# Kernel optimization log

Hardware: AMD Instinct MI355X
Metric: run time of the kernel (lower is better)

Reference implementation:

```python
import jax, jax.numpy as jnp
import numpy as np

SP, WD, H, HID = 8, 3, 8, 256
D = HID // H
TEMP = 0.1


def setup_inputs() -> dict:
    key = jax.random.key(0)
    ks = jax.random.split(key, 14)
    B, Lq, Lk, F = 4, 1024, 2048, SP + WD
    s = 0.05
    return {
        "q_fp": jax.random.normal(ks[0], (B, Lq, F), jnp.float32),
        "v_ret": jax.random.normal(ks[1], (B, Lk, F), jnp.float32),
        "pi_star": jax.random.uniform(ks[2], (B, Lq, Lk), jnp.float32),
        "Wq_s": jax.random.normal(ks[3], (HID, SP), jnp.float32) * s,
        "bq_s": jax.random.normal(ks[4], (HID,), jnp.float32) * s,
        "Wk_s": jax.random.normal(ks[5], (HID, SP), jnp.float32) * s,
        "bk_s": jax.random.normal(ks[6], (HID,), jnp.float32) * s,
        "Wq_w": jax.random.normal(ks[7], (HID, WD), jnp.float32) * s,
        "bq_w": jax.random.normal(ks[8], (HID,), jnp.float32) * s,
        "Wk_w": jax.random.normal(ks[9], (HID, WD), jnp.float32) * s,
        "bk_w": jax.random.normal(ks[10], (HID,), jnp.float32) * s,
        "Wv": jax.random.normal(ks[11], (HID, F), jnp.float32) * s,
        "bv": jnp.zeros((HID,), jnp.float32),
        "Wo": jax.random.normal(ks[12], (HID, HID), jnp.float32) * s,
        "bo": jnp.zeros((HID,), jnp.float32),
        "wave_blend": jnp.array(0.5, jnp.float32),
    }


def _proj(x, W, b):
    # x: [B, L, F_in] -> [B, H, L, D]
    B, L, _ = x.shape
    return (x @ W.T + b).reshape(B, L, H, D).transpose(0, 2, 1, 3)


def reference(q_fp, v_ret, pi_star, Wq_s, bq_s, Wk_s, bk_s, Wq_w, bq_w, Wk_w, bk_w, Wv, bv, Wo, bo, wave_blend):
    B, Lq, _ = q_fp.shape
    # split streams: first SP dims spatial, next WD dims wave (F == SP+WD)
    q_sp, q_wv = q_fp[..., :SP], q_fp[..., SP:SP + WD]
    k_sp, k_wv = v_ret[..., :SP], v_ret[..., SP:SP + WD]
    # structural branch: scaled dot product
    q_struct = _proj(q_sp, Wq_s, bq_s)
    k_struct = _proj(k_sp, Wk_s, bk_s)
    spatial_logits = jnp.einsum('bhqd,bhkd->bhqk', q_struct, k_struct) / np.float32(np.sqrt(D))
    # wave branch: negative squared euclidean distance via norm expansion
    q_wp = _proj(q_wv, Wq_w, bq_w)
    k_wp = _proj(k_wv, Wk_w, bk_w)
    qn = jnp.sum(q_wp * q_wp, axis=-1)[..., :, None]   # [B,H,Lq,1]
    kn = jnp.sum(k_wp * k_wp, axis=-1)[..., None, :]   # [B,H,1,Lk]
    qk = jnp.einsum('bhqd,bhkd->bhqk', q_wp, k_wp)
    wave_logits = -(qn + kn - 2.0 * qk) / np.float32(TEMP)
    alpha = jax.nn.sigmoid(wave_blend)
    transport_mask = jnp.log(jnp.clip(pi_star, 1e-9, None))[:, None]  # [B,1,Lq,Lk]
    attn = jax.nn.softmax((1.0 - alpha) * spatial_logits + alpha * wave_logits + transport_mask, axis=-1)
    values = _proj(v_ret, Wv, bv)  # [B,H,Lk,D]
    ctx = jnp.einsum('bhqk,bhkd->bhqd', attn, values)
    ctx = ctx.transpose(0, 2, 1, 3).reshape(B, Lq, HID)
    return ctx @ Wo.T + bo
```

## Files before the change

kernel.cpp:

```cpp
#include <hip/hip_runtime.h>
#include <hip/hip_bf16.h>
#include <cstdint>

#define B_    4
#define LQ    1024
#define LK    2048
#define FEAT  11
#define SP_   8
#define WD_   3
#define H_    8
#define HID_  256
#define LOG2E 1.4426950408889634f
#define SPLIT 4
#define KPS   (LK / SPLIT)
#define ITERS (KPS / 64)

typedef __attribute__((ext_vector_type(4))) float f32x4;
typedef __attribute__((ext_vector_type(8))) short bf16x8;
typedef __attribute__((ext_vector_type(4))) short s16x4;

__device__ __forceinline__ float sigmoidf_(float x) { return 1.f / (1.f + __expf(-x)); }

__device__ __forceinline__ short f2bf(float f) {
  unsigned u = __float_as_uint(f);
  u += 0x7fffu + ((u >> 16) & 1u);
  return (short)(u >> 16);
}
__device__ __forceinline__ float bf2f(short s) {
  return __uint_as_float(((unsigned)(unsigned short)s) << 16);
}

__device__ __forceinline__ void gl_lds16(const void* g, void* l) {
  __builtin_amdgcn_global_load_lds(
      (const __attribute__((address_space(1))) unsigned int*)g,
      (__attribute__((address_space(3))) unsigned int*)l, 16, 0, 0);
}

__global__ __launch_bounds__(256) void proj_q_kernel(
    const float* __restrict__ q_fp, const float* __restrict__ Wq_s,
    const float* __restrict__ bq_s, const float* __restrict__ Wq_w,
    const float* __restrict__ bq_w, const float* __restrict__ wb,
    short* __restrict__ Qh)
{
  const int row = blockIdx.x;
  const int t   = threadIdx.x;
  const float alpha = sigmoidf_(wb[0]);
  const float c1 = (1.f - alpha) * 0.17677669529663687f * LOG2E;
  const float c2 = 2.f * alpha * 10.f * LOG2E;

  const float* x = q_fp + (size_t)row * FEAT;
  float xs[FEAT];
  #pragma unroll
  for (int f = 0; f < FEAT; ++f) xs[f] = x[f];

  float s = bq_s[t];
  #pragma unroll
  for (int f = 0; f < SP_; ++f) s += xs[f] * Wq_s[t * SP_ + f];
  float w = bq_w[t];
  #pragma unroll
  for (int f = 0; f < WD_; ++f) w += xs[SP_ + f] * Wq_w[t * WD_ + f];

  const int h = t >> 5, d = t & 31;
  const int b = row >> 10, q = row & (LQ - 1);
  const size_t base = ((size_t)(b * H_ + h) * LQ + q) * 64;
  Qh[base + d]      = f2bf(c1 * s);
  Qh[base + 32 + d] = f2bf(c2 * w);
}

__global__ __launch_bounds__(256) void projk_pack_kernel(
    const float* __restrict__ v_ret, const float* __restrict__ Wk_s,
    const float* __restrict__ bk_s, const float* __restrict__ Wk_w,
    const float* __restrict__ bk_w, const float* __restrict__ Wv,
    const float* __restrict__ bv,   const float* __restrict__ wb,
    short* __restrict__ KV, float* __restrict__ kb)
{
  __shared__ float ldsv[64][33];
  const int blk = blockIdx.x, bh = blockIdx.y;
  const int b = bh >> 3, h = bh & 7;
  const int t = threadIdx.x;
  const int kl = t >> 2, part = t & 3;
  const int k = blk * 64 + kl;
  const float alpha = sigmoidf_(wb[0]);

  const float* x = v_ret + (size_t)(b * LK + k) * FEAT;
  float xs[FEAT];
  #pragma unroll
  for (int f = 0; f < FEAT; ++f) xs[f] = x[f];

  float s8[8], w8[8], v8[8];
  #pragma unroll
  for (int i = 0; i < 8; ++i) {
    const int d = h * 32 + part * 8 + i;
    float s = bk_s[d];
    #pragma unroll
    for (int f = 0; f < SP_; ++f) s += xs[f] * Wk_s[d * SP_ + f];
    float w = bk_w[d];
    #pragma unroll
    for (int f = 0; f < WD_; ++f) w += xs[SP_ + f] * Wk_w[d * WD_ + f];
    float v = bv[d];
    #pragma unroll
    for (int f = 0; f < FEAT; ++f) v += xs[f] * Wv[d * FEAT + f];
    s8[i] = s; w8[i] = w; v8[i] = v;
    ldsv[kl][part * 8 + i] = v;
  }

  float sq = 0.f;
  #pragma unroll
  for (int i = 0; i < 8; ++i) sq += w8[i] * w8[i];
  sq += __shfl_xor(sq, 1);
  sq += __shfl_xor(sq, 2);
  if (part == 0) kb[(size_t)bh * LK + k] = -10.f * alpha * LOG2E * sq;

  const int a  = kl >> 5;
  const int bb = (kl >> 2) & 1;
  const int p  = kl - a * 32 - bb * 4;
  const int lo = ((p >> 3) << 2) | (p & 3);
  const int t4 = a * 2 + bb;
  const size_t base = ((size_t)bh * 32 + blk) * 768;

  bf16x8 hs, hw;
  #pragma unroll
  for (int i = 0; i < 8; ++i) { hs[i] = f2bf(s8[i]); hw[i] = f2bf(w8[i]); }
  *(bf16x8*)(KV + (base + (t4 * 2 + 0) * 64 + part * 16 + lo) * 8) = hs;
  *(bf16x8*)(KV + (base + (t4 * 2 + 1) * 64 + part * 16 + lo) * 8) = hw;

  __syncthreads();

  {
    const int j = t >> 6, l = t & 63;
    const int dt = j >> 1, kw = j & 1;
    const int lo2 = l & 15, quad = l >> 4;
    const int d = dt * 16 + lo2;
    bf16x8 hv;
    #pragma unroll
    for (int i = 0; i < 8; ++i)
      hv[i] = f2bf(ldsv[kw * 32 + quad * 8 + i][d]);
    *(bf16x8*)(KV + (base + 512 + t) * 8) = hv;
  }
}

__global__ __launch_bounds__(256) void pi_prepack_kernel(
    const float* __restrict__ pi, float* __restrict__ piP)
{
  const int Gid = blockIdx.x * 256 + threadIdx.x;
  const int g    = Gid & 255;
  const int kblk = (Gid >> 8) & 31;
  const int qt   = (Gid >> 13) & 63;
  const int b    = Gid >> 19;
  const int t4 = g >> 6, l = g & 63;
  const int lo = l & 15, quad = l >> 4;
  const int q = qt * 16 + lo;
  const int k = kblk * 64 + ((t4 >> 1) << 5) + ((t4 & 1) << 2) + quad * 8;
  const f32x4 v = *(const f32x4*)(pi + ((size_t)(b * LQ + q) * LK + k));
  *(f32x4*)(piP + (size_t)Gid * 4) = v;
}

union PF { int i[4]; bf16x8 v; };

__device__ __forceinline__ void attn_step2(
    const short* __restrict__ cbuf, const bf16x8 qh[2][2],
    const float* __restrict__ pib0, const float* __restrict__ pib1,
    const float* __restrict__ kbp, const bf16x8 ones, int lane,
    float m[2], f32x4 o[2][2], f32x4 ol[2])
{
  f32x4 pi4[2][4];
  #pragma unroll
  for (int t4 = 0; t4 < 4; ++t4) {
    pi4[0][t4] = *(const f32x4*)(pib0 + t4 * 256);
    pi4[1][t4] = *(const f32x4*)(pib1 + t4 * 256);
  }
  f32x4 kb4[4];
  kb4[0] = *(const f32x4*)(kbp);
  kb4[1] = *(const f32x4*)(kbp + 4);
  kb4[2] = *(const f32x4*)(kbp + 32);
  kb4[3] = *(const f32x4*)(kbp + 36);

  f32x4 st[2][4];
  #pragma unroll
  for (int t4 = 0; t4 < 4; ++t4) {
    const bf16x8 ka0 = *(const bf16x8*)(cbuf + ((t4 * 2 + 0) * 64 + lane) * 8);
    const bf16x8 ka1 = *(const bf16x8*)(cbuf + ((t4 * 2 + 1) * 64 + lane) * 8);
    #pragma unroll
    for (int tl = 0; tl < 2; ++tl) {
      f32x4 z = {0.f, 0.f, 0.f, 0.f};
      z = __builtin_amdgcn_mfma_f32_16x16x32_bf16(ka0, qh[tl][0], z, 0, 0, 0);
      z = __builtin_amdgcn_mfma_f32_16x16x32_bf16(ka1, qh[tl][1], z, 0, 0, 0);
      st[tl][t4] = z;
    }
  }

  const bf16x8 va00 = *(const bf16x8*)(cbuf + ((512 + 0 * 64) + lane) * 8);
  const bf16x8 va01 = *(const bf16x8*)(cbuf + ((512 + 1 * 64) + lane) * 8);
  const bf16x8 va10 = *(const bf16x8*)(cbuf + ((512 + 2 * 64) + lane) * 8);
  const bf16x8 va11 = *(const bf16x8*)(cbuf + ((512 + 3 * 64) + lane) * 8);

  #pragma unroll
  for (int tl = 0; tl < 2; ++tl) {
    float lg[16];
    #pragma unroll
    for (int t4 = 0; t4 < 4; ++t4) {
      #pragma unroll
      for (int r = 0; r < 4; ++r) lg[t4 * 4 + r] = st[tl][t4][r] + kb4[t4][r];
    }

    float cm = lg[0];
    #pragma unroll
    for (int j = 1; j < 16; ++j) cm = fmaxf(cm, lg[j]);
    cm = fmaxf(cm, __shfl_xor(cm, 16));
    cm = fmaxf(cm, __shfl_xor(cm, 32));
    const float mn = fmaxf(m[tl], cm);
    const float sc = __builtin_amdgcn_exp2f(m[tl] - mn);
    m[tl] = mn;

    unsigned eu[16];
    #pragma unroll
    for (int t4 = 0; t4 < 4; ++t4) {
      #pragma unroll
      for (int r = 0; r < 4; ++r)
        eu[t4 * 4 + r] = __float_as_uint(
            __builtin_amdgcn_exp2f(lg[t4 * 4 + r] - mn) * pi4[tl][t4][r]);
    }

    PF pf0, pf1;
    #pragma unroll
    for (int p = 0; p < 4; ++p) {
      pf0.i[p] = __builtin_amdgcn_perm(eu[2 * p + 1], eu[2 * p], 0x07060302u);
      pf1.i[p] = __builtin_amdgcn_perm(eu[8 + 2 * p + 1], eu[8 + 2 * p], 0x07060302u);
    }

    #pragma unroll
    for (int r = 0; r < 4; ++r) { o[tl][0][r] *= sc; o[tl][1][r] *= sc; ol[tl][r] *= sc; }

    o[tl][0] = __builtin_amdgcn_mfma_f32_16x16x32_bf16(va00, pf0.v, o[tl][0], 0, 0, 0);
    o[tl][0] = __builtin_amdgcn_mfma_f32_16x16x32_bf16(va01, pf1.v, o[tl][0], 0, 0, 0);
    o[tl][1] = __builtin_amdgcn_mfma_f32_16x16x32_bf16(va10, pf0.v, o[tl][1], 0, 0, 0);
    o[tl][1] = __builtin_amdgcn_mfma_f32_16x16x32_bf16(va11, pf1.v, o[tl][1], 0, 0, 0);
    ol[tl] = __builtin_amdgcn_mfma_f32_16x16x32_bf16(ones, pf0.v, ol[tl], 0, 0, 0);
    ol[tl] = __builtin_amdgcn_mfma_f32_16x16x32_bf16(ones, pf1.v, ol[tl], 0, 0, 0);
  }
}

__global__ __launch_bounds__(256, 4) void attn_kernel(
    const short* __restrict__ Qh, const short* __restrict__ KV,
    const float* __restrict__ kb, const float* __restrict__ piP,
    float* __restrict__ part)
{
  __shared__ short skv[2][6144];
  const int id = blockIdx.x;
  const int combo = id & 127;
  const int qblk  = id >> 7;
  const int bh = combo >> 2;
  const int sp = combo & 3;
  const int b = bh >> 3;
  const int wv = threadIdx.x >> 6;
  const int lane = threadIdx.x & 63;
  const int lo16 = lane & 15;
  const int quad = lane >> 4;
  const int qt0 = qblk * 8 + wv * 2;
  const int blk0 = sp * ITERS;

  bf16x8 qh[2][2];
  #pragma unroll
  for (int tl = 0; tl < 2; ++tl) {
    const size_t qoff = ((size_t)bh * LQ + (qt0 + tl) * 16 + lo16) * 64 + quad * 8;
    qh[tl][0] = *(const bf16x8*)(Qh + qoff);
    qh[tl][1] = *(const bf16x8*)(Qh + qoff + 32);
  }

  const float* pib0 = piP + (((size_t)(b * 64 + qt0) * 32 + blk0) << 10) + lane * 4;
  const float* pib1 = piP + (((size_t)(b * 64 + qt0 + 1) * 32 + blk0) << 10) + lane * 4;
  const float* kbbase = kb + (size_t)bh * LK + sp * KPS + quad * 8;

  bf16x8 ones;
  #pragma unroll
  for (int j = 0; j < 8; ++j) ones[j] = (lo16 == 0) ? (short)0x3F80 : (short)0;

  float m[2] = {-1e30f, -1e30f};
  f32x4 o[2][2] = {{{0.f,0.f,0.f,0.f},{0.f,0.f,0.f,0.f}},
                   {{0.f,0.f,0.f,0.f},{0.f,0.f,0.f,0.f}}};
  f32x4 ol[2] = {{0.f,0.f,0.f,0.f},{0.f,0.f,0.f,0.f}};

  {
    const size_t gb = ((size_t)bh * 32 + blk0) * 768;
    #pragma unroll
    for (int c = 0; c < 3; ++c)
      gl_lds16(KV + (gb + c * 256 + wv * 64 + lane) * 8,
               &skv[0][c * 2048 + wv * 512]);
  }

  for (int it = 0; it < ITERS; it += 2) {
    __syncthreads();
    {
      const size_t gb = ((size_t)bh * 32 + blk0 + it + 1) * 768;
      #pragma unroll
      for (int c = 0; c < 3; ++c)
        gl_lds16(KV + (gb + c * 256 + wv * 64 + lane) * 8,
                 &skv[1][c * 2048 + wv * 512]);
    }
    attn_step2(skv[0], qh, pib0 + ((size_t)it << 10), pib1 + ((size_t)it << 10),
               kbbase + it * 64, ones, lane, m, o, ol);

    __syncthreads();
    if (it + 2 < ITERS) {
      const size_t gb = ((size_t)bh * 32 + blk0 + it + 2) * 768;
      #pragma unroll
      for (int c = 0; c < 3; ++c)
        gl_lds16(KV + (gb + c * 256 + wv * 64 + lane) * 8,
                 &skv[0][c * 2048 + wv * 512]);
    }
    attn_step2(skv[1], qh, pib0 + ((size_t)(it + 1) << 10), pib1 + ((size_t)(it + 1) << 10),
               kbbase + (it + 1) * 64, ones, lane, m, o, ol);
  }

  #pragma unroll
  for (int tl = 0; tl < 2; ++tl) {
    const int q = (qt0 + tl) * 16 + lo16;
    float* ppart = part + ((size_t)(sp * 32 + bh) * LQ + q) * 36;
    if (quad == 0) { ppart[0] = m[tl]; ppart[1] = ol[tl][0]; }
    *(f32x4*)(ppart + 4 + quad * 4)  = o[tl][0];
    *(f32x4*)(ppart + 20 + quad * 4) = o[tl][1];
  }
}

__global__ __launch_bounds__(256) void wo_prep_kernel(
    const float* __restrict__ Wo, short* __restrict__ WoH, short* __restrict__ WoL)
{
  const int i = (blockIdx.x * 256 + threadIdx.x) * 4;
  const f32x4 v = *(const f32x4*)(Wo + i);
  s16x4 h, l;
  #pragma unroll
  for (int j = 0; j < 4; ++j) {
    h[j] = f2bf(v[j]);
    l[j] = f2bf(v[j] - bf2f(h[j]));
  }
  *(s16x4*)(WoH + i) = h;
  *(s16x4*)(WoL + i) = l;
}

__global__ __launch_bounds__(256) void out_kernel(
    const float* __restrict__ part, const short* __restrict__ WoH,
    const short* __restrict__ WoL, const float* __restrict__ bo,
    float* __restrict__ out)
{
  const int t = threadIdx.x;
  const int wv = t >> 6, lane = t & 63;
  const int lo16 = lane & 15, quad = lane >> 4;
  const int mt = blockIdx.x;
  const size_t gq = (size_t)mt * 16 + lo16;
  const int b = (int)(gq >> 10), qq = (int)(gq & (LQ - 1));

  bf16x8 Ah[8], Al[8];
  #pragma unroll
  for (int win = 0; win < 8; ++win) {
    const size_t r = (size_t)(b * H_ + win) * LQ + qq;
    const float* p[SPLIT];
    float ms[SPLIT], ls[SPLIT];
    #pragma unroll
    for (int s = 0; s < SPLIT; ++s) {
      p[s] = part + (r + (size_t)s * (B_ * H_ * LQ)) * 36;
      ms[s] = p[s][0]; ls[s] = p[s][1];
    }
    float mM = ms[0];
    #pragma unroll
    for (int s = 1; s < SPLIT; ++s) mM = fmaxf(mM, ms[s]);
    float ws[SPLIT], den = 0.f;
    #pragma unroll
    for (int s = 0; s < SPLIT; ++s) {
      ws[s] = __builtin_amdgcn_exp2f(ms[s] - mM);
      den += ws[s] * ls[s];
    }
    const float inv = 1.f / den;

    float c8[8];
    #pragma unroll
    for (int j = 0; j < 8; ++j) c8[j] = 0.f;
    #pragma unroll
    for (int s = 0; s < SPLIT; ++s) {
      const f32x4 a0 = *(const f32x4*)(p[s] + 4 + quad * 8);
      const f32x4 a1 = *(const f32x4*)(p[s] + 8 + quad * 8);
      #pragma unroll
      for (int j = 0; j < 4; ++j) {
        c8[j]     += ws[s] * a0[j];
        c8[4 + j] += ws[s] * a1[j];
      }
    }
    #pragma unroll
    for (int j = 0; j < 8; ++j) {
      const float cv = c8[j] * inv;
      const short hi = f2bf(cv);
      Ah[win][j] = hi;
      Al[win][j] = f2bf(cv - bf2f(hi));
    }
  }

  const int n0 = wv * 64;
  #pragma unroll
  for (int nt = 0; nt < 4; ++nt) {
    const int nb = n0 + nt * 16;
    const short* bh = WoH + (size_t)(nb + lo16) * HID_ + quad * 8;
    const short* bl = WoL + (size_t)(nb + lo16) * HID_ + quad * 8;
    const float bias = bo[nb + lo16];
    f32x4 acc = {bias, bias, bias, bias};
    #pragma unroll
    for (int win = 0; win < 8; ++win) {
      const bf16x8 Bh = *(const bf16x8*)(bh + win * 32);
      const bf16x8 Bl = *(const bf16x8*)(bl + win * 32);
      acc = __builtin_amdgcn_mfma_f32_16x16x32_bf16(Ah[win], Bh, acc, 0, 0, 0);
      acc = __builtin_amdgcn_mfma_f32_16x16x32_bf16(Al[win], Bh, acc, 0, 0, 0);
      acc = __builtin_amdgcn_mfma_f32_16x16x32_bf16(Ah[win], Bl, acc, 0, 0, 0);
    }
    #pragma unroll
    for (int r4 = 0; r4 < 4; ++r4)
      out[(size_t)(mt * 16 + quad * 4 + r4) * HID_ + nb + lo16] = acc[r4];
  }
}

extern "C" void kernel_launch(void* const* d_in, const int* in_sizes, int n_in,
                              void* d_out, int out_size, void* d_ws, size_t ws_size,
                              hipStream_t stream)
{
  const float* q_fp  = (const float*)d_in[0];
  const float* v_ret = (const float*)d_in[1];
  const float* pi    = (const float*)d_in[2];
  const float* Wq_s  = (const float*)d_in[3];
  const float* bq_s  = (const float*)d_in[4];
  const float* Wk_s  = (const float*)d_in[5];
  const float* bk_s  = (const float*)d_in[6];
  const float* Wq_w  = (const float*)d_in[7];
  const float* bq_w  = (const float*)d_in[8];
  const float* Wk_w  = (const float*)d_in[9];
  const float* bk_w  = (const float*)d_in[10];
  const float* Wv    = (const float*)d_in[11];
  const float* bv    = (const float*)d_in[12];
  const float* Wo    = (const float*)d_in[13];
  const float* bo    = (const float*)d_in[14];
  const float* wb    = (const float*)d_in[15];
  float* out = (float*)d_out;

  short* Qh   = (short*)d_ws;
  short* KV   = Qh + (size_t)2097152;
  float* kbuf = (float*)(KV + (size_t)6291456);
  float* piP  = kbuf + (size_t)65536;
  float* part = piP + (size_t)8388608;
  short* WoH  = (short*)piP;
  short* WoL  = WoH + (size_t)65536;

  proj_q_kernel<<<B_ * LQ, 256, 0, stream>>>(q_fp, Wq_s, bq_s, Wq_w, bq_w, wb, Qh);
  projk_pack_kernel<<<dim3(LK / 64, 32), 256, 0, stream>>>(
      v_ret, Wk_s, bk_s, Wk_w, bk_w, Wv, bv, wb, KV, kbuf);
  pi_prepack_kernel<<<8192, 256, 0, stream>>>(pi, piP);
  attn_kernel<<<(LQ / 128) * 32 * SPLIT, 256, 0, stream>>>(Qh, KV, kbuf, piP, part);
  wo_prep_kernel<<<64, 256, 0, stream>>>(Wo, WoH, WoL);
  out_kernel<<<(B_ * LQ) / 16, 256, 0, stream>>>(part, WoH, WoL, bo, out);
}
```

Baseline: 181.6 us.

## Read pi directly in attention kernel and vectorize Q projection stores

```diff
diff --git a/kernel.cpp b/kernel.cpp
--- a/kernel.cpp
+++ b/kernel.cpp
@@ -42,29 +42,38 @@
     const float* __restrict__ bq_w, const float* __restrict__ wb,
     short* __restrict__ Qh)
 {
-  const int row = blockIdx.x;
-  const int t   = threadIdx.x;
+  const int blk = blockIdx.x, bh = blockIdx.y;
+  const int b = bh >> 3, h = bh & 7;
+  const int t = threadIdx.x;
+  const int ql = t >> 2, part = t & 3;
+  const int q = blk * 64 + ql;
   const float alpha = sigmoidf_(wb[0]);
   const float c1 = (1.f - alpha) * 0.17677669529663687f * LOG2E;
   const float c2 = 2.f * alpha * 10.f * LOG2E;
 
-  const float* x = q_fp + (size_t)row * FEAT;
+  const float* x = q_fp + (size_t)(b * LQ + q) * FEAT;
   float xs[FEAT];
   #pragma unroll
   for (int f = 0; f < FEAT; ++f) xs[f] = x[f];
 
-  float s = bq_s[t];
-  #pragma unroll
-  for (int f = 0; f < SP_; ++f) s += xs[f] * Wq_s[t * SP_ + f];
-  float w = bq_w[t];
-  #pragma unroll
-  for (int f = 0; f < WD_; ++f) w += xs[SP_ + f] * Wq_w[t * WD_ + f];
-
-  const int h = t >> 5, d = t & 31;
-  const int b = row >> 10, q = row & (LQ - 1);
-  const size_t base = ((size_t)(b * H_ + h) * LQ + q) * 64;
-  Qh[base + d]      = f2bf(c1 * s);
-  Qh[base + 32 + d] = f2bf(c2 * w);
+  const size_t base = ((size_t)bh * LQ + q) * 64 + part * 8;
+  s16x4 out_s[2], out_w[2];
+  #pragma unroll
+  for (int i = 0; i < 8; ++i) {
+    const int dg = h * 32 + part * 8 + i;
+    float s = bq_s[dg];
+    #pragma unroll
+    for (int f = 0; f < SP_; ++f) s += xs[f] * Wq_s[dg * SP_ + f];
+    float w = bq_w[dg];
+    #pragma unroll
+    for (int f = 0; f < WD_; ++f) w += xs[SP_ + f] * Wq_w[dg * WD_ + f];
+    out_s[i >> 2][i & 3] = f2bf(c1 * s);
+    out_w[i >> 2][i & 3] = f2bf(c2 * w);
+  }
+  *(s16x4*)(Qh + base)          = out_s[0];
+  *(s16x4*)(Qh + base + 4)      = out_s[1];
+  *(s16x4*)(Qh + base + 32)     = out_w[0];
+  *(s16x4*)(Qh + base + 36)     = out_w[1];
 }
 
 __global__ __launch_bounds__(256) void projk_pack_kernel(
@@ -139,22 +148,6 @@
   }
 }
 
-__global__ __launch_bounds__(256) void pi_prepack_kernel(
-    const float* __restrict__ pi, float* __restrict__ piP)
-{
-  const int Gid = blockIdx.x * 256 + threadIdx.x;
-  const int g    = Gid & 255;
-  const int kblk = (Gid >> 8) & 31;
-  const int qt   = (Gid >> 13) & 63;
-  const int b    = Gid >> 19;
-  const int t4 = g >> 6, l = g & 63;
-  const int lo = l & 15, quad = l >> 4;
-  const int q = qt * 16 + lo;
-  const int k = kblk * 64 + ((t4 >> 1) << 5) + ((t4 & 1) << 2) + quad * 8;
-  const f32x4 v = *(const f32x4*)(pi + ((size_t)(b * LQ + q) * LK + k));
-  *(f32x4*)(piP + (size_t)Gid * 4) = v;
-}
-
 union PF { int i[4]; bf16x8 v; };
 
 __device__ __forceinline__ void attn_step2(
@@ -164,11 +157,14 @@
     float m[2], f32x4 o[2][2], f32x4 ol[2])
 {
   f32x4 pi4[2][4];
-  #pragma unroll
-  for (int t4 = 0; t4 < 4; ++t4) {
-    pi4[0][t4] = *(const f32x4*)(pib0 + t4 * 256);
-    pi4[1][t4] = *(const f32x4*)(pib1 + t4 * 256);
-  }
+  pi4[0][0] = *(const f32x4*)(pib0);
+  pi4[0][1] = *(const f32x4*)(pib0 + 4);
+  pi4[0][2] = *(const f32x4*)(pib0 + 32);
+  pi4[0][3] = *(const f32x4*)(pib0 + 36);
+  pi4[1][0] = *(const f32x4*)(pib1);
+  pi4[1][1] = *(const f32x4*)(pib1 + 4);
+  pi4[1][2] = *(const f32x4*)(pib1 + 32);
+  pi4[1][3] = *(const f32x4*)(pib1 + 36);
   f32x4 kb4[4];
   kb4[0] = *(const f32x4*)(kbp);
   kb4[1] = *(const f32x4*)(kbp + 4);
@@ -242,7 +238,7 @@
 
 __global__ __launch_bounds__(256, 4) void attn_kernel(
     const short* __restrict__ Qh, const short* __restrict__ KV,
-    const float* __restrict__ kb, const float* __restrict__ piP,
+    const float* __restrict__ kb, const float* __restrict__ pi,
     float* __restrict__ part)
 {
   __shared__ short skv[2][6144];
@@ -267,8 +263,9 @@
     qh[tl][1] = *(const bf16x8*)(Qh + qoff + 32);
   }
 
-  const float* pib0 = piP + (((size_t)(b * 64 + qt0) * 32 + blk0) << 10) + lane * 4;
-  const float* pib1 = piP + (((size_t)(b * 64 + qt0 + 1) * 32 + blk0) << 10) + lane * 4;
+  const float* pib0 = pi + ((size_t)(b * LQ + qt0 * 16 + lo16)) * LK
+                      + sp * KPS + quad * 8;
+  const float* pib1 = pib0 + (size_t)16 * LK;
   const float* kbbase = kb + (size_t)bh * LK + sp * KPS + quad * 8;
 
   bf16x8 ones;
@@ -297,7 +294,7 @@
         gl_lds16(KV + (gb + c * 256 + wv * 64 + lane) * 8,
                  &skv[1][c * 2048 + wv * 512]);
     }
-    attn_step2(skv[0], qh, pib0 + ((size_t)it << 10), pib1 + ((size_t)it << 10),
+    attn_step2(skv[0], qh, pib0 + it * 64, pib1 + it * 64,
                kbbase + it * 64, ones, lane, m, o, ol);
 
     __syncthreads();
@@ -308,7 +305,7 @@
         gl_lds16(KV + (gb + c * 256 + wv * 64 + lane) * 8,
                  &skv[0][c * 2048 + wv * 512]);
     }
-    attn_step2(skv[1], qh, pib0 + ((size_t)(it + 1) << 10), pib1 + ((size_t)(it + 1) << 10),
+    attn_step2(skv[1], qh, pib0 + (it + 1) * 64, pib1 + (it + 1) * 64,
                kbbase + (it + 1) * 64, ones, lane, m, o, ol);
   }
 
@@ -440,16 +437,15 @@
   short* Qh   = (short*)d_ws;
   short* KV   = Qh + (size_t)2097152;
   float* kbuf = (float*)(KV + (size_t)6291456);
-  float* piP  = kbuf + (size_t)65536;
-  float* part = piP + (size_t)8388608;
-  short* WoH  = (short*)piP;
+  float* part = kbuf + (size_t)65536;
+  short* WoH  = (short*)(part + (size_t)4718592);
   short* WoL  = WoH + (size_t)65536;
 
-  proj_q_kernel<<<B_ * LQ, 256, 0, stream>>>(q_fp, Wq_s, bq_s, Wq_w, bq_w, wb, Qh);
+  proj_q_kernel<<<dim3(LQ / 64, 32), 256, 0, stream>>>(
+      q_fp, Wq_s, bq_s, Wq_w, bq_w, wb, Qh);
   projk_pack_kernel<<<dim3(LK / 64, 32), 256, 0, stream>>>(
       v_ret, Wk_s, bk_s, Wk_w, bk_w, Wv, bv, wb, KV, kbuf);
-  pi_prepack_kernel<<<8192, 256, 0, stream>>>(pi, piP);
-  attn_kernel<<<(LQ / 128) * 32 * SPLIT, 256, 0, stream>>>(Qh, KV, kbuf, piP, part);
+  attn_kernel<<<(LQ / 128) * 32 * SPLIT, 256, 0, stream>>>(Qh, KV, kbuf, pi, part);
   wo_prep_kernel<<<64, 256, 0, stream>>>(Wo, WoH, WoL);
   out_kernel<<<(B_ * LQ) / 16, 256, 0, stream>>>(part, WoH, WoL, bo, out);
 }
```

Result: no change. 183.2 us (+0.9%).
